# Kernel optimization log

Measured on AMD Instinct MI355X. Metric: run time of the kernel, lower is better.

The kernel has to match this reference:

```python
import jax, jax.numpy as jnp
import numpy as np

N_NODES = 50000

# DGL ChebConv with k=2 and the standard lambda_max=2 approximation:
#   L_hat = L - I = -D^{-1/2} A D^{-1/2}
#   X0 = X ; X1 = L_hat @ X ; out = concat([X0, X1], -1) @ W + b
# Norm uses in-degrees (DGL behavior).

def setup_inputs() -> dict:
    key = jax.random.key(0)
    ks = jax.random.split(key, 8)
    E = 800000
    src = jax.random.randint(ks[0], (E,), 0, N_NODES, dtype=jnp.int32)
    dst = jax.random.randint(ks[1], (E,), 0, N_NODES, dtype=jnp.int32)
    def w(k, shape):
        fan_in = shape[0]
        return jax.random.normal(k, shape, jnp.float32) * (1.0 / np.sqrt(fan_in))
    return {
        "x": jax.random.normal(ks[2], (N_NODES, 128), jnp.float32),
        "src": src, "dst": dst,
        "W1": w(ks[3], (256, 256)), "b1": jnp.zeros((256,), jnp.float32),
        "W2": w(ks[4], (512, 256)), "b2": jnp.zeros((256,), jnp.float32),
        "W3": w(ks[5], (512, 128)), "b3": jnp.zeros((128,), jnp.float32),
    }

def _cheb_layer(h, src, dst, dinv, W, b):
    # X1 = -D^{-1/2} A D^{-1/2} h  (lambda_max = 2)
    hn = h * dinv[:, None]
    agg = jax.ops.segment_sum(hn[src], dst, num_segments=N_NODES)
    x1 = -(agg * dinv[:, None])
    return jnp.concatenate([h, x1], axis=-1) @ W + b

def reference(x, src, dst, W1, b1, W2, b2, W3, b3):
    deg = jax.ops.segment_sum(jnp.ones_like(dst, dtype=x.dtype), dst,
                              num_segments=N_NODES)
    dinv = jnp.where(deg > 0, jax.lax.rsqrt(jnp.maximum(deg, 1.0)), 0.0)
    h = jnp.tanh(_cheb_layer(x, src, dst, dinv, W1, b1))
    for _ in range(3):  # hid_layer = 3
        h = jnp.tanh(_cheb_layer(h, src, dst, dinv, W2, b2))
    return _cheb_layer(h, src, dst, dinv, W3, b3)
```

## Files before the change

kernel.cpp:

```cpp
#include <hip/hip_runtime.h>
#include <cmath>

#define NN 50000
#define CAP 64

typedef short v8s __attribute__((ext_vector_type(8)));
typedef float v4f __attribute__((ext_vector_type(4)));

__device__ __forceinline__ float b2f(unsigned short u) {
    return __uint_as_float(((unsigned int)u) << 16);
}
__device__ __forceinline__ unsigned short f2b(float f) {
    unsigned int x = __float_as_uint(f);
    x += 0x7fffu + ((x >> 16) & 1u);
    return (unsigned short)(x >> 16);
}

__device__ __forceinline__ void gld16(const void* g, void* l) {
    __builtin_amdgcn_global_load_lds(
        (const __attribute__((address_space(1))) unsigned int*)g,
        (__attribute__((address_space(3))) unsigned int*)l, 16, 0, 0);
}

__global__ void sniff_kernel(const unsigned short* __restrict__ x, int* __restrict__ mode) {
    __shared__ int c2[2];
    int t = threadIdx.x;
    unsigned int e = (x[t] >> 7) & 0xFFu;
    unsigned long long m = __ballot(e >= 100u && e <= 140u);
    if ((t & 63) == 0) c2[t >> 6] = __popcll(m);
    __syncthreads();
    if (t == 0) *mode = (c2[0] + c2[1] >= 112) ? 0 : 1;
}

__global__ void fill_kernel(const int* __restrict__ src, const int* __restrict__ dst,
                            int* __restrict__ cnt, unsigned short* __restrict__ ell, int E) {
    int e = blockIdx.x * blockDim.x + threadIdx.x;
    if (e < E) {
        int d = dst[e];
        int pos = atomicAdd(&cnt[d], 1);
        if (pos < CAP) ell[d * CAP + pos] = (unsigned short)src[e];
    }
}

__global__ void dinv_kernel(const int* __restrict__ cnt, float* __restrict__ dinv, int n) {
    int i = blockIdx.x * blockDim.x + threadIdx.x;
    if (i < n) {
        int d = cnt[i];
        dinv[i] = (d > 0) ? rsqrtf((float)d) : 0.0f;
    }
}

__global__ void prep_kernel(const void* __restrict__ x,
                            const void* __restrict__ W1, const void* __restrict__ W2,
                            const void* __restrict__ W3, const void* __restrict__ b1,
                            const void* __restrict__ b2, const void* __restrict__ b3,
                            unsigned short* __restrict__ buf,
                            unsigned short* __restrict__ WT1, unsigned short* __restrict__ WT2,
                            unsigned short* __restrict__ WT3, unsigned short* __restrict__ bb1,
                            unsigned short* __restrict__ bb2, unsigned short* __restrict__ bb3,
                            unsigned short* __restrict__ bbz,
                            const int* __restrict__ modep) {
    int mode = *modep;
    int b = blockIdx.x, t = threadIdx.x;
    if (b < 3125) {
        int idx = b * 256 + t;
        int n = idx >> 4, c = idx & 15;
        if (mode == 0) {
            ((uint4*)buf)[n * 64 + c] = ((const uint4*)x)[idx];
        } else {
            const float* xf = (const float*)x + (size_t)idx * 8;
            unsigned short o[8];
#pragma unroll
            for (int i = 0; i < 8; ++i) o[i] = f2b(xf[i]);
            ((uint4*)buf)[n * 64 + c] = *(const uint4*)o;
        }
    } else if (b < 3381) {
        int idx = (b - 3125) * 256 + t;
        int n = idx >> 8, k = idx & 255;
        WT1[idx] = mode ? f2b(((const float*)W1)[k * 256 + n])
                        : ((const unsigned short*)W1)[k * 256 + n];
    } else if (b < 3893) {
        int idx = (b - 3381) * 256 + t;
        int n = idx >> 9, k = idx & 511;
        WT2[idx] = mode ? f2b(((const float*)W2)[k * 256 + n])
                        : ((const unsigned short*)W2)[k * 256 + n];
    } else if (b < 4149) {
        int idx = (b - 3893) * 256 + t;
        int n = idx >> 9, k = idx & 511;
        WT3[idx] = mode ? f2b(((const float*)W3)[k * 128 + n])
                        : ((const unsigned short*)W3)[k * 128 + n];
    } else {
        if (t < 256) {
            bb1[t] = mode ? f2b(((const float*)b1)[t]) : ((const unsigned short*)b1)[t];
            bb2[t] = mode ? f2b(((const float*)b2)[t]) : ((const unsigned short*)b2)[t];
        }
        if (t < 128) {
            bb3[t] = mode ? f2b(((const float*)b3)[t]) : ((const unsigned short*)b3)[t];
            bbz[t] = 0;
        }
    }
}

template <int FPL>
__global__ void spmm_kernel(const unsigned short* __restrict__ h, int ldh,
                            const int* __restrict__ cnt, const unsigned short* __restrict__ ell,
                            const float* __restrict__ dinv,
                            unsigned short* __restrict__ out, int ldo) {
    int node = blockIdx.x * 4 + (threadIdx.x >> 6);
    int lane = threadIdx.x & 63;
    int c = cnt[node]; c = (c < CAP) ? c : CAP;
    int sl = (int)ell[node * CAP + lane];
    float dl = dinv[sl];
    float acc[FPL];
#pragma unroll
    for (int i = 0; i < FPL; ++i) acc[i] = 0.f;
    const int col = lane * FPL;

    int g = 0;
    for (; g + 8 <= c; g += 8) {
        int s[8]; float d[8];
#pragma unroll
        for (int i = 0; i < 8; ++i) { s[i] = __shfl(sl, g + i); d[i] = __shfl(dl, g + i); }
        if (FPL == 4) {
            ushort4 v[8];
#pragma unroll
            for (int i = 0; i < 8; ++i)
                v[i] = *(const ushort4*)(h + (size_t)s[i] * ldh + col);
#pragma unroll
            for (int i = 0; i < 8; ++i) {
                acc[0] += d[i] * b2f(v[i].x); acc[1] += d[i] * b2f(v[i].y);
                acc[2] += d[i] * b2f(v[i].z); acc[3] += d[i] * b2f(v[i].w);
            }
        } else {
            ushort2 v[8];
#pragma unroll
            for (int i = 0; i < 8; ++i)
                v[i] = *(const ushort2*)(h + (size_t)s[i] * ldh + col);
#pragma unroll
            for (int i = 0; i < 8; ++i) {
                acc[0] += d[i] * b2f(v[i].x); acc[1] += d[i] * b2f(v[i].y);
            }
        }
    }
    for (; g < c; ++g) {
        int sg = __shfl(sl, g);
        float dg = __shfl(dl, g);
        const unsigned short* hp = h + (size_t)sg * ldh + col;
        if (FPL == 4) {
            ushort4 v = *(const ushort4*)hp;
            acc[0] += dg * b2f(v.x); acc[1] += dg * b2f(v.y);
            acc[2] += dg * b2f(v.z); acc[3] += dg * b2f(v.w);
        } else {
            ushort2 v = *(const ushort2*)hp;
            acc[0] += dg * b2f(v.x); acc[1] += dg * b2f(v.y);
        }
    }

    float dn = -dinv[node];
    unsigned short* op = out + (size_t)node * ldo + col;
    if (FPL == 4) {
        ushort4 o;
        o.x = f2b(acc[0] * dn); o.y = f2b(acc[1] * dn);
        o.z = f2b(acc[2] * dn); o.w = f2b(acc[3] * dn);
        *(ushort4*)op = o;
    } else {
        ushort2 o;
        o.x = f2b(acc[0] * dn); o.y = f2b(acc[1] * dn);
        *(ushort2*)op = o;
    }
}

template <int K32, int NQ, int LDW, int KW0, bool ADDV>
__global__ void __launch_bounds__(2 * NQ * 64)
gemm_lds_kernel(const unsigned short* __restrict__ A, int lda,
                const unsigned short* __restrict__ WT,
                const unsigned short* __restrict__ bias,
                const unsigned short* __restrict__ addv, int ldav,
                void* __restrict__ out, int ldo,
                int M, int dotanh, int is_final, const int* __restrict__ modep) {
    constexpr int NB   = NQ * 64;
    constexpr int NTHR = 2 * NQ * 64;
    constexpr int ACH  = 128 * 4;
    constexpr int BCH  = NB * 4;
    constexpr int ROUNDS = (ACH + BCH) / NTHR;
    constexpr int LDSZ  = (128 + NB) * 32;
    __shared__ unsigned short lds[2 * LDSZ];

    const int tid = threadIdx.x;
    const int wave = tid >> 6, lane = tid & 63, quad = lane >> 4, l16 = lane & 15;
    const int mh = wave / NQ, nq = wave % NQ;
    const int m0 = blockIdx.x * 128;

    v4f acc[4][4];
#pragma unroll
    for (int mi = 0; mi < 4; ++mi)
#pragma unroll
        for (int ni = 0; ni < 4; ++ni) acc[mi][ni] = (v4f){0.f, 0.f, 0.f, 0.f};

    const unsigned short* gp[ROUNDS];
#pragma unroll
    for (int r = 0; r < ROUNDS; ++r) {
        int c = tid + r * NTHR;
        if (c < ACH) {
            int row = m0 + (c >> 2);
            if (row >= M) row = M - 1;
            gp[r] = A + (size_t)row * lda + (c & 3) * 8;
        } else {
            int cb = c - ACH;
            gp[r] = WT + (size_t)(cb >> 2) * LDW + KW0 + (cb & 3) * 8;
        }
    }

    auto STAGE = [&](int bsel, int k0) {
#pragma unroll
        for (int r = 0; r < ROUNDS; ++r) {
            int c = tid + r * NTHR;
            gld16(gp[r] + k0, (void*)&lds[bsel * LDSZ + c * 8]);
        }
    };

    STAGE(0, 0);
#pragma unroll 1
    for (int t = 0; t < K32; ++t) {
        if (t + 1 < K32) {
            STAGE((t + 1) & 1, (t + 1) * 32);
            asm volatile("s_waitcnt vmcnt(%0)" :: "i"(ROUNDS) : "memory");
        } else {
            asm volatile("s_waitcnt vmcnt(0)" ::: "memory");
        }
        __builtin_amdgcn_s_barrier();

        const unsigned short* aT = &lds[(t & 1) * LDSZ];
        const unsigned short* bT = aT + 128 * 32;
        v8s a_frag[4], b_frag[4];
#pragma unroll
        for (int mi = 0; mi < 4; ++mi)
            a_frag[mi] = *(const v8s*)&aT[(mh * 64 + mi * 16 + l16) * 32 + quad * 8];
#pragma unroll
        for (int ni = 0; ni < 4; ++ni)
            b_frag[ni] = *(const v8s*)&bT[(nq * 64 + ni * 16 + l16) * 32 + quad * 8];
#pragma unroll
        for (int mi = 0; mi < 4; ++mi)
#pragma unroll
            for (int ni = 0; ni < 4; ++ni)
                acc[mi][ni] = __builtin_amdgcn_mfma_f32_16x16x32_bf16(a_frag[mi], b_frag[ni],
                                                                      acc[mi][ni], 0, 0, 0);
        asm volatile("s_waitcnt lgkmcnt(0)" ::: "memory");
        __builtin_amdgcn_s_barrier();
    }

    int fin = is_final ? *modep : 0;
#pragma unroll
    for (int ni = 0; ni < 4; ++ni) {
        int colc = nq * 64 + ni * 16 + l16;
        float bv = b2f(bias[colc]);
#pragma unroll
        for (int mi = 0; mi < 4; ++mi) {
#pragma unroll
            for (int r = 0; r < 4; ++r) {
                int row = m0 + mh * 64 + mi * 16 + quad * 4 + r;
                if (row < M) {
                    float v = acc[mi][ni][r] + bv;
                    if constexpr (ADDV) v += b2f(addv[(size_t)row * ldav + colc]);
                    if (dotanh) v = tanhf(v);
                    if (fin) ((float*)out)[(size_t)row * ldo + colc] = v;
                    else     ((unsigned short*)out)[(size_t)row * ldo + colc] = f2b(v);
                }
            }
        }
    }
}

static inline size_t al256(size_t x) { return (x + 255) & ~(size_t)255; }

extern "C" void kernel_launch(void* const* d_in, const int* in_sizes, int n_in,
                              void* d_out, int out_size, void* d_ws, size_t ws_size,
                              hipStream_t stream) {
    const void* x  = d_in[0];
    const int* src = (const int*)d_in[1];
    const int* dst = (const int*)d_in[2];
    const void* W1 = d_in[3]; const void* b1 = d_in[4];
    const void* W2 = d_in[5]; const void* b2 = d_in[6];
    const void* W3 = d_in[7]; const void* b3 = d_in[8];
    const int E = in_sizes[1];

    char* p = (char*)d_ws;
    int* mode     = (int*)p;            p += 256;
    int* cnt      = (int*)p;            p += al256((size_t)NN * 4);
    float* dinv   = (float*)p;          p += al256((size_t)NN * 4);
    unsigned short* ell = (unsigned short*)p; p += al256((size_t)NN * CAP * 2);
    unsigned short* WT1 = (unsigned short*)p; p += al256((size_t)256 * 256 * 2);
    unsigned short* WT2 = (unsigned short*)p; p += al256((size_t)256 * 512 * 2);
    unsigned short* WT3 = (unsigned short*)p; p += al256((size_t)128 * 512 * 2);
    unsigned short* bb1 = (unsigned short*)p; p += al256((size_t)256 * 2);
    unsigned short* bb2 = (unsigned short*)p; p += al256((size_t)256 * 2);
    unsigned short* bb3 = (unsigned short*)p; p += al256((size_t)128 * 2);
    unsigned short* bbz = (unsigned short*)p; p += al256((size_t)128 * 2);
    unsigned short* buf = (unsigned short*)p; p += al256((size_t)NN * 512 * 2);

    hipMemsetAsync(cnt, 0, (size_t)NN * 4, stream);
    sniff_kernel<<<1, 128, 0, stream>>>((const unsigned short*)x, mode);
    prep_kernel<<<4150, 256, 0, stream>>>(x, W1, W2, W3, b1, b2, b3,
                                          buf, WT1, WT2, WT3, bb1, bb2, bb3, bbz, mode);
    int eb = (E + 255) / 256;
    fill_kernel<<<eb, 256, 0, stream>>>(src, dst, cnt, ell, E);
    dinv_kernel<<<(NN + 255) / 256, 256, 0, stream>>>(cnt, dinv, NN);

    const int SPMM_GRID = NN / 4;
    const int GB = (NN + 127) / 128;

    spmm_kernel<2><<<SPMM_GRID, 256, 0, stream>>>(buf, 512, cnt, ell, dinv, buf + 128, 512);
    gemm_lds_kernel<8, 4, 256, 0, false><<<GB, 512, 0, stream>>>(
        buf, 512, WT1, bb1, nullptr, 0, buf, 512, NN, 1, 0, mode);
    spmm_kernel<4><<<SPMM_GRID, 256, 0, stream>>>(buf, 512, cnt, ell, dinv, buf + 256, 512);
    gemm_lds_kernel<16, 4, 512, 0, false><<<GB, 512, 0, stream>>>(
        buf, 512, WT2, bb2, nullptr, 0, buf, 512, NN, 1, 0, mode);
    spmm_kernel<4><<<SPMM_GRID, 256, 0, stream>>>(buf, 512, cnt, ell, dinv, buf + 256, 512);
    gemm_lds_kernel<16, 4, 512, 0, false><<<GB, 512, 0, stream>>>(
        buf, 512, WT2, bb2, nullptr, 0, buf, 512, NN, 1, 0, mode);
    spmm_kernel<4><<<SPMM_GRID, 256, 0, stream>>>(buf, 512, cnt, ell, dinv, buf + 256, 512);
    gemm_lds_kernel<16, 4, 512, 0, false><<<GB, 512, 0, stream>>>(
        buf, 512, WT2, bb2, nullptr, 0, buf, 512, NN, 1, 0, mode);
    gemm_lds_kernel<8, 2, 512, 256, false><<<GB, 256, 0, stream>>>(
        buf, 512, WT3, bbz, nullptr, 0, buf + 256, 512, NN, 0, 0, mode);
    spmm_kernel<2><<<SPMM_GRID, 256, 0, stream>>>(buf + 256, 512, cnt, ell, dinv,
                                                  buf + 384, 512);
    gemm_lds_kernel<8, 2, 512, 0, true><<<GB, 256, 0, stream>>>(
        buf, 512, WT3, bb3, buf + 384, 512, d_out, 128, NN, 0, 1, mode);
}
```

Before: 540.3 us.

## Overlap hidden-layer SpMM with the X0 half of the GEMM in one launch

For the three hidden layers, a combined kernel runs two kinds of blocks in one grid. The first GB blocks compute h@W[:256] and write fp32 partials to a new workspace buffer. The remaining blocks do the neighbour aggregation that produces X1. A second GEMM then computes X1@W[256:] and adds the fp32 partials, bias and tanh. This lets the memory-bound gather run alongside the MFMA work, at the cost of an extra fp32 round-trip through global memory and one more launch per layer.

```diff
diff --git a/kernel.cpp b/kernel.cpp
--- a/kernel.cpp
+++ b/kernel.cpp
@@ -170,12 +170,12 @@
     }
 }
 
-template <int K32, int NQ, int LDW, int KW0, bool ADDV>
+template <int K32, int NQ, int LDW, int KW0, int AV>
 __global__ void __launch_bounds__(2 * NQ * 64)
 gemm_lds_kernel(const unsigned short* __restrict__ A, int lda,
                 const unsigned short* __restrict__ WT,
                 const unsigned short* __restrict__ bias,
-                const unsigned short* __restrict__ addv, int ldav,
+                const void* __restrict__ addv, int ldav,
                 void* __restrict__ out, int ldo,
                 int M, int dotanh, int is_final, const int* __restrict__ modep) {
     constexpr int NB   = NQ * 64;
@@ -261,13 +261,148 @@
                 int row = m0 + mh * 64 + mi * 16 + quad * 4 + r;
                 if (row < M) {
                     float v = acc[mi][ni][r] + bv;
-                    if constexpr (ADDV) v += b2f(addv[(size_t)row * ldav + colc]);
+                    if constexpr (AV == 1)
+                        v += b2f(((const unsigned short*)addv)[(size_t)row * ldav + colc]);
+                    if constexpr (AV == 2)
+                        v += ((const float*)addv)[(size_t)row * ldav + colc];
                     if (dotanh) v = tanhf(v);
                     if (fin) ((float*)out)[(size_t)row * ldo + colc] = v;
                     else     ((unsigned short*)out)[(size_t)row * ldo + colc] = f2b(v);
                 }
             }
         }
+    }
+}
+
+template <int K32, int NQ, int LDW, int KW0>
+__global__ void __launch_bounds__(512)
+fused_kernel(const unsigned short* __restrict__ h, int lda,
+             const unsigned short* __restrict__ WT,
+             float* __restrict__ ztop, int ldz, int GB, int M,
+             const int* __restrict__ cnt, const unsigned short* __restrict__ ell,
+             const float* __restrict__ dinv,
+             unsigned short* __restrict__ x1out, int ldo1) {
+    constexpr int NB   = NQ * 64;
+    constexpr int NTHR = 2 * NQ * 64;
+    constexpr int ACH  = 128 * 4;
+    constexpr int BCH  = NB * 4;
+    constexpr int ROUNDS = (ACH + BCH) / NTHR;
+    constexpr int LDSZ  = (128 + NB) * 32;
+    __shared__ unsigned short lds[2 * LDSZ];
+
+    if ((int)blockIdx.x < GB) {
+        const int tid = threadIdx.x;
+        const int wave = tid >> 6, lane = tid & 63, quad = lane >> 4, l16 = lane & 15;
+        const int mh = wave / NQ, nq = wave % NQ;
+        const int m0 = blockIdx.x * 128;
+
+        v4f acc[4][4];
+#pragma unroll
+        for (int mi = 0; mi < 4; ++mi)
+#pragma unroll
+            for (int ni = 0; ni < 4; ++ni) acc[mi][ni] = (v4f){0.f, 0.f, 0.f, 0.f};
+
+        const unsigned short* gp[ROUNDS];
+#pragma unroll
+        for (int r = 0; r < ROUNDS; ++r) {
+            int c = tid + r * NTHR;
+            if (c < ACH) {
+                int row = m0 + (c >> 2);
+                if (row >= M) row = M - 1;
+                gp[r] = h + (size_t)row * lda + (c & 3) * 8;
+            } else {
+                int cb = c - ACH;
+                gp[r] = WT + (size_t)(cb >> 2) * LDW + KW0 + (cb & 3) * 8;
+            }
+        }
+
+        auto STAGE = [&](int bsel, int k0) {
+#pragma unroll
+            for (int r = 0; r < ROUNDS; ++r) {
+                int c = tid + r * NTHR;
+                gld16(gp[r] + k0, (void*)&lds[bsel * LDSZ + c * 8]);
+            }
+        };
+
+        STAGE(0, 0);
+#pragma unroll 1
+        for (int t = 0; t < K32; ++t) {
+            if (t + 1 < K32) {
+                STAGE((t + 1) & 1, (t + 1) * 32);
+                asm volatile("s_waitcnt vmcnt(%0)" :: "i"(ROUNDS) : "memory");
+            } else {
+                asm volatile("s_waitcnt vmcnt(0)" ::: "memory");
+            }
+            __builtin_amdgcn_s_barrier();
+
+            const unsigned short* aT = &lds[(t & 1) * LDSZ];
+            const unsigned short* bT = aT + 128 * 32;
+            v8s a_frag[4], b_frag[4];
+#pragma unroll
+            for (int mi = 0; mi < 4; ++mi)
+                a_frag[mi] = *(const v8s*)&aT[(mh * 64 + mi * 16 + l16) * 32 + quad * 8];
+#pragma unroll
+            for (int ni = 0; ni < 4; ++ni)
+                b_frag[ni] = *(const v8s*)&bT[(nq * 64 + ni * 16 + l16) * 32 + quad * 8];
+#pragma unroll
+            for (int mi = 0; mi < 4; ++mi)
+#pragma unroll
+                for (int ni = 0; ni < 4; ++ni)
+                    acc[mi][ni] = __builtin_amdgcn_mfma_f32_16x16x32_bf16(
+                        a_frag[mi], b_frag[ni], acc[mi][ni], 0, 0, 0);
+            asm volatile("s_waitcnt lgkmcnt(0)" ::: "memory");
+            __builtin_amdgcn_s_barrier();
+        }
+
+#pragma unroll
+        for (int ni = 0; ni < 4; ++ni) {
+            int colc = nq * 64 + ni * 16 + l16;
+#pragma unroll
+            for (int mi = 0; mi < 4; ++mi) {
+#pragma unroll
+                for (int r = 0; r < 4; ++r) {
+                    int row = m0 + mh * 64 + mi * 16 + quad * 4 + r;
+                    if (row < M) ztop[(size_t)row * ldz + colc] = acc[mi][ni][r];
+                }
+            }
+        }
+    } else {
+        int node = ((int)blockIdx.x - GB) * 8 + (threadIdx.x >> 6);
+        int lane = threadIdx.x & 63;
+        if (node >= NN) return;
+        int c = cnt[node]; c = (c < CAP) ? c : CAP;
+        int sl = (int)ell[node * CAP + lane];
+        float dl = dinv[sl];
+        float a0 = 0.f, a1 = 0.f, a2 = 0.f, a3 = 0.f;
+        const int col = lane * 4;
+
+        int g = 0;
+        for (; g + 8 <= c; g += 8) {
+            int s[8]; float d[8];
+#pragma unroll
+            for (int i = 0; i < 8; ++i) { s[i] = __shfl(sl, g + i); d[i] = __shfl(dl, g + i); }
+            ushort4 v[8];
+#pragma unroll
+            for (int i = 0; i < 8; ++i)
+                v[i] = *(const ushort4*)(h + (size_t)s[i] * lda + col);
+#pragma unroll
+            for (int i = 0; i < 8; ++i) {
+                a0 += d[i] * b2f(v[i].x); a1 += d[i] * b2f(v[i].y);
+                a2 += d[i] * b2f(v[i].z); a3 += d[i] * b2f(v[i].w);
+            }
+        }
+        for (; g < c; ++g) {
+            int sg = __shfl(sl, g);
+            float dg = __shfl(dl, g);
+            ushort4 v = *(const ushort4*)(h + (size_t)sg * lda + col);
+            a0 += dg * b2f(v.x); a1 += dg * b2f(v.y);
+            a2 += dg * b2f(v.z); a3 += dg * b2f(v.w);
+        }
+        float dn = -dinv[node];
+        ushort4 o;
+        o.x = f2b(a0 * dn); o.y = f2b(a1 * dn);
+        o.z = f2b(a2 * dn); o.w = f2b(a3 * dn);
+        *(ushort4*)(x1out + (size_t)node * ldo1 + col) = o;
     }
 }
 
@@ -297,6 +432,8 @@
     unsigned short* bb3 = (unsigned short*)p; p += al256((size_t)128 * 2);
     unsigned short* bbz = (unsigned short*)p; p += al256((size_t)128 * 2);
     unsigned short* buf = (unsigned short*)p; p += al256((size_t)NN * 512 * 2);
+    float* ztop   = (float*)p;          p += al256((size_t)NN * 256 * 4);
+    bool can_fuse = ((size_t)(p - (char*)d_ws) <= ws_size);
 
     hipMemsetAsync(cnt, 0, (size_t)NN * 4, stream);
     sniff_kernel<<<1, 128, 0, stream>>>((const unsigned short*)x, mode);
@@ -308,23 +445,30 @@
 
     const int SPMM_GRID = NN / 4;
     const int GB = (NN + 127) / 128;
+    const int SB = (NN + 7) / 8;
 
     spmm_kernel<2><<<SPMM_GRID, 256, 0, stream>>>(buf, 512, cnt, ell, dinv, buf + 128, 512);
-    gemm_lds_kernel<8, 4, 256, 0, false><<<GB, 512, 0, stream>>>(
+    gemm_lds_kernel<8, 4, 256, 0, 0><<<GB, 512, 0, stream>>>(
         buf, 512, WT1, bb1, nullptr, 0, buf, 512, NN, 1, 0, mode);
-    spmm_kernel<4><<<SPMM_GRID, 256, 0, stream>>>(buf, 512, cnt, ell, dinv, buf + 256, 512);
-    gemm_lds_kernel<16, 4, 512, 0, false><<<GB, 512, 0, stream>>>(
-        buf, 512, WT2, bb2, nullptr, 0, buf, 512, NN, 1, 0, mode);
-    spmm_kernel<4><<<SPMM_GRID, 256, 0, stream>>>(buf, 512, cnt, ell, dinv, buf + 256, 512);
-    gemm_lds_kernel<16, 4, 512, 0, false><<<GB, 512, 0, stream>>>(
-        buf, 512, WT2, bb2, nullptr, 0, buf, 512, NN, 1, 0, mode);
-    spmm_kernel<4><<<SPMM_GRID, 256, 0, stream>>>(buf, 512, cnt, ell, dinv, buf + 256, 512);
-    gemm_lds_kernel<16, 4, 512, 0, false><<<GB, 512, 0, stream>>>(
-        buf, 512, WT2, bb2, nullptr, 0, buf, 512, NN, 1, 0, mode);
-    gemm_lds_kernel<8, 2, 512, 256, false><<<GB, 256, 0, stream>>>(
+
+    for (int l = 0; l < 3; ++l) {
+        if (can_fuse) {
+            fused_kernel<8, 4, 512, 0><<<GB + SB, 512, 0, stream>>>(
+                buf, 512, WT2, ztop, 256, GB, NN, cnt, ell, dinv, buf + 256, 512);
+            gemm_lds_kernel<8, 4, 512, 256, 2><<<GB, 512, 0, stream>>>(
+                buf + 256, 512, WT2, bb2, ztop, 256, buf, 512, NN, 1, 0, mode);
+        } else {
+            spmm_kernel<4><<<SPMM_GRID, 256, 0, stream>>>(buf, 512, cnt, ell, dinv,
+                                                          buf + 256, 512);
+            gemm_lds_kernel<16, 4, 512, 0, 0><<<GB, 512, 0, stream>>>(
+                buf, 512, WT2, bb2, nullptr, 0, buf, 512, NN, 1, 0, mode);
+        }
+    }
+
+    gemm_lds_kernel<8, 2, 512, 256, 0><<<GB, 256, 0, stream>>>(
         buf, 512, WT3, bbz, nullptr, 0, buf + 256, 512, NN, 0, 0, mode);
     spmm_kernel<2><<<SPMM_GRID, 256, 0, stream>>>(buf + 256, 512, cnt, ell, dinv,
                                                   buf + 384, 512);
-    gemm_lds_kernel<8, 2, 512, 0, true><<<GB, 256, 0, stream>>>(
+    gemm_lds_kernel<8, 2, 512, 0, 1><<<GB, 256, 0, stream>>>(
         buf, 512, WT3, bb3, buf + 384, 512, d_out, 128, NN, 0, 1, mode);
 }
```

Result: slower. 651.9 us (+20.7%).
